# Optimization experiments

Measured on AMD Instinct MI355X. Metric: run time of the kernel, lower is better.

The kernel has to match this reference:

```python
import jax, jax.numpy as jnp
import numpy as np

SEQ, BATCH, IN_DIM, HID, OUT = 512, 256, 300, 256, 2


def setup_inputs() -> dict:
    key = jax.random.key(0)
    ks = jax.random.split(key, 7)
    s_ih = 1.0 / np.sqrt(HID)
    return {
        "x": jax.random.normal(ks[0], (SEQ, BATCH, IN_DIM), jnp.float32),
        "W_ih": jax.random.uniform(ks[1], (HID, IN_DIM), jnp.float32, -s_ih, s_ih),
        "W_hh": jax.random.uniform(ks[2], (HID, HID), jnp.float32, -s_ih, s_ih),
        "b_ih": jax.random.uniform(ks[3], (HID,), jnp.float32, -s_ih, s_ih),
        "b_hh": jax.random.uniform(ks[4], (HID,), jnp.float32, -s_ih, s_ih),
        "W_fc": jax.random.uniform(ks[5], (OUT, HID), jnp.float32, -s_ih, s_ih),
        "b_fc": jax.random.uniform(ks[6], (OUT,), jnp.float32, -s_ih, s_ih),
    }


def reference(x, W_ih, W_hh, b_ih, b_hh, W_fc, b_fc):
    # Precompute input projection for all timesteps at once: [T, B, H]
    xp = jnp.einsum('tbi,hi->tbh', x, W_ih) + b_ih + b_hh

    def step(h, xt):
        h_new = jnp.tanh(xt + h @ W_hh.T)
        return h_new, None

    h0 = jnp.zeros((x.shape[1], W_hh.shape[0]), x.dtype)
    hT, _ = jax.lax.scan(step, h0, xp)  # hT: [B, H]
    # Dropout(0.3) is identity in eval mode.
    logits = hT @ W_fc.T + b_fc  # [B, 2]
    return jax.nn.log_softmax(logits, axis=-1)
```

## Files before the change

### kernel.cpp

```cpp
#include <hip/hip_runtime.h>
#include <hip/hip_bf16.h>
#include <cstdint>
#include <cstddef>

#define SEQ 512
#define BATCH 256
#define IN_DIM 300
#define HID 256

typedef __attribute__((ext_vector_type(8))) short bf16x8;
typedef __attribute__((ext_vector_type(4))) float f32x4;

__device__ __forceinline__ unsigned short f2bf(float f) {
  union { float f; unsigned int u; } v; v.f = f;
  unsigned int u = v.u;
  return (unsigned short)((u + 0x7fffu + ((u >> 16) & 1u)) >> 16);
}
__device__ __forceinline__ unsigned short f2bf_fast(float f) {
  union { float f; unsigned int u; } v; v.f = f;
  return (unsigned short)((v.u + 0x8000u) >> 16);
}
__device__ __forceinline__ float bitsf(unsigned int u) {
  union { unsigned int u; float f; } v; v.u = u; return v.f;
}
__device__ __forceinline__ bf16x8 cvt8(float a0,float a1,float a2,float a3,
                                       float a4,float a5,float a6,float a7) {
  union { __hip_bfloat162 h2[4]; bf16x8 v; } c;
  c.h2[0] = __float22bfloat162_rn(make_float2(a0, a1));
  c.h2[1] = __float22bfloat162_rn(make_float2(a2, a3));
  c.h2[2] = __float22bfloat162_rn(make_float2(a4, a5));
  c.h2[3] = __float22bfloat162_rn(make_float2(a6, a7));
  return c.v;
}

__global__ __launch_bounds__(256) void conv_wih(const float* __restrict__ w,
                                                unsigned short* __restrict__ w_bf) {
  int idx = blockIdx.x * 256 + threadIdx.x;
  int n = idx / 320, k = idx - n * 320;
  float v = (k < IN_DIM) ? w[n * IN_DIM + k] : 0.f;
  w_bf[idx] = f2bf(v);
}

__global__ __launch_bounds__(256) void gemm_xp(const float* __restrict__ x,
    const unsigned short* __restrict__ w_bf, const float* __restrict__ b_ih,
    const float* __restrict__ b_hh, unsigned short* __restrict__ xp2)
{
  __shared__ unsigned short a_lds[64][40];
  __shared__ unsigned short w_lds[256][40];
  const int tid  = threadIdx.x;
  const int wave = tid >> 6;
  const int lane = tid & 63;
  const int l15  = lane & 15;
  const int quad = lane >> 4;
  const long m0 = (long)blockIdx.x * 64;

  f32x4 acc[4][4];
  #pragma unroll
  for (int mt = 0; mt < 4; ++mt)
    #pragma unroll
    for (int nt = 0; nt < 4; ++nt) acc[mt][nt] = (f32x4){0.f, 0.f, 0.f, 0.f};

  const int ar = tid >> 2;
  const int ac = (tid & 3) * 8;

  for (int kc = 0; kc < 10; ++kc) {
    const int k0 = kc * 32;
    {
      float v[8];
      const float* src = x + (size_t)(m0 + ar) * IN_DIM + (k0 + ac);
      if (k0 + ac + 8 <= IN_DIM) {
        float2 p0 = *(const float2*)(src + 0);
        float2 p1 = *(const float2*)(src + 2);
        float2 p2 = *(const float2*)(src + 4);
        float2 p3 = *(const float2*)(src + 6);
        v[0]=p0.x; v[1]=p0.y; v[2]=p1.x; v[3]=p1.y;
        v[4]=p2.x; v[5]=p2.y; v[6]=p3.x; v[7]=p3.y;
      } else {
        #pragma unroll
        for (int j = 0; j < 8; ++j) v[j] = (k0 + ac + j < IN_DIM) ? src[j] : 0.f;
      }
      *(bf16x8*)&a_lds[ar][ac] = cvt8(v[0],v[1],v[2],v[3],v[4],v[5],v[6],v[7]);
    }
    #pragma unroll
    for (int i = 0; i < 8; ++i) {
      int e = tid + i * 256;
      int n = e >> 3;
      int kk = (e & 7) * 4;
      uint2 d = *(const uint2*)(w_bf + n * 320 + k0 + kk);
      *(uint2*)&w_lds[n][kk] = d;
    }
    __syncthreads();
    bf16x8 afr[4], bfr[4];
    #pragma unroll
    for (int mt = 0; mt < 4; ++mt)
      afr[mt] = *(const bf16x8*)&a_lds[mt*16 + l15][quad*8];
    #pragma unroll
    for (int nt = 0; nt < 4; ++nt)
      bfr[nt] = *(const bf16x8*)&w_lds[wave*64 + nt*16 + l15][quad*8];
    #pragma unroll
    for (int mt = 0; mt < 4; ++mt)
      #pragma unroll
      for (int nt = 0; nt < 4; ++nt)
        acc[mt][nt] = __builtin_amdgcn_mfma_f32_16x16x32_bf16(afr[mt], bfr[nt], acc[mt][nt], 0, 0, 0);
    __syncthreads();
  }
  const int t = (int)(blockIdx.x >> 2);
  #pragma unroll
  for (int nt = 0; nt < 4; ++nt) {
    const int n = wave*64 + nt*16 + l15;
    const float kb = 2.0f * (b_ih[n] + b_hh[n]);
    const int tid_s = (wave*2 + (nt>>1))*64 + (nt&1)*32 + (quad&1)*16 + l15;
    #pragma unroll
    for (int mt = 0; mt < 4; ++mt) {
      const int g = ((int)(blockIdx.x & 3))*8 + mt*2 + (quad>>1);
      float y0 = fmaf(2.0f, acc[mt][nt][0], kb);
      float y1 = fmaf(2.0f, acc[mt][nt][1], kb);
      float y2 = fmaf(2.0f, acc[mt][nt][2], kb);
      float y3 = fmaf(2.0f, acc[mt][nt][3], kb);
      union { __hip_bfloat162 h2[2]; uint2 u; } pk;
      pk.h2[0] = __float22bfloat162_rn(make_float2(y0, y1));
      pk.h2[1] = __float22bfloat162_rn(make_float2(y2, y3));
      *(uint2*)(xp2 + (((size_t)t*32 + g)*512 + tid_s)*4) = pk.u;
    }
  }
}

__global__ __launch_bounds__(512) void rnn_scan(const float* __restrict__ W_hh,
    const unsigned short* __restrict__ xp2, float* __restrict__ hT)
{
  __shared__ unsigned short hbuf[2][8 * 264];
  const int tid  = threadIdx.x;
  const int wave = tid >> 6;
  const int lane = tid & 63;
  const int l15  = lane & 15;
  const int quad = lane >> 4;
  const int g = blockIdx.x;
  const int c0 = wave * 32;

  bf16x8 wf[2][8];
  #pragma unroll
  for (int nt = 0; nt < 2; ++nt) {
    const int n = c0 + nt*16 + l15;
    #pragma unroll
    for (int kc = 0; kc < 8; ++kc) {
      const float* src = W_hh + n*HID + kc*32 + quad*8;
      float4 p0 = *(const float4*)src;
      float4 p1 = *(const float4*)(src + 4);
      wf[nt][kc] = cvt8(p0.x,p0.y,p0.z,p0.w,p1.x,p1.y,p1.z,p1.w);
    }
  }

  const int myrow = ((lane >> 4) & 1) * 4;
  const int mycol = c0 + ((lane >> 5) << 4) + l15;
  const int b = g * 8 + myrow;

  for (int i = tid; i < 8 * 264; i += 512) hbuf[0][i] = 0;

  const unsigned short* xbase = xp2 + (((size_t)g) * 512 + tid) * 4;

  __syncthreads();

  uint2 xq[16];
  for (int tc = 0; tc < SEQ / 16; ++tc) {
    const unsigned short* pb = xbase + (size_t)tc * 16 * 65536;
    #pragma unroll
    for (int j = 0; j < 16; ++j)
      xq[j] = *(const uint2*)(pb + (size_t)j * 65536);
    #pragma unroll
    for (int j = 0; j < 16; ++j) {
      const int t = tc * 16 + j;
      const int cur = j & 1;
      bf16x8 afr[8];
      #pragma unroll
      for (int kc = 0; kc < 8; ++kc)
        afr[kc] = *(const bf16x8*)&hbuf[cur][(l15 & 7) * 264 + kc*32 + quad*8];
      f32x4 acc0 = (f32x4){0.f,0.f,0.f,0.f};
      f32x4 acc1 = (f32x4){0.f,0.f,0.f,0.f};
      #pragma unroll
      for (int kc = 0; kc < 8; ++kc) {
        acc0 = __builtin_amdgcn_mfma_f32_16x16x32_bf16(afr[kc], wf[0][kc], acc0, 0, 0, 0);
        acc1 = __builtin_amdgcn_mfma_f32_16x16x32_bf16(afr[kc], wf[1][kc], acc1, 0, 0, 0);
      }
      float xv[4];
      xv[0] = bitsf(xq[j].x << 16);
      xv[1] = bitsf(xq[j].x & 0xffff0000u);
      xv[2] = bitsf(xq[j].y << 16);
      xv[3] = bitsf(xq[j].y & 0xffff0000u);
      #pragma unroll
      for (int r = 0; r < 4; ++r) {
        float sel = (lane < 32) ? acc0[r] : acc1[r];
        float y  = fmaf(2.0f, sel, xv[r]);
        float e  = __expf(y);
        float hv = fmaf(-2.0f, __builtin_amdgcn_rcpf(e + 1.0f), 1.0f);
        if (t < SEQ - 1)
          hbuf[1 - cur][(myrow + r) * 264 + mycol] = f2bf_fast(hv);
        else
          hT[(size_t)(b + r) * HID + mycol] = hv;
      }
      __syncthreads();
    }
  }
}

__global__ __launch_bounds__(64) void fc_head(const float* __restrict__ hT,
    const float* __restrict__ W_fc, const float* __restrict__ b_fc,
    float* __restrict__ out)
{
  const int b = blockIdx.x;
  const int l = threadIdx.x;
  float s0 = 0.f, s1 = 0.f;
  #pragma unroll
  for (int j0 = 0; j0 < HID; j0 += 64) {
    float h = hT[(size_t)b * HID + j0 + l];
    s0 += h * W_fc[j0 + l];
    s1 += h * W_fc[HID + j0 + l];
  }
  #pragma unroll
  for (int off = 32; off > 0; off >>= 1) {
    s0 += __shfl_xor(s0, off, 64);
    s1 += __shfl_xor(s1, off, 64);
  }
  if (l == 0) {
    float l0 = s0 + b_fc[0], l1 = s1 + b_fc[1];
    float m = fmaxf(l0, l1);
    float lse = m + logf(expf(l0 - m) + expf(l1 - m));
    out[b*2 + 0] = l0 - lse;
    out[b*2 + 1] = l1 - lse;
  }
}

extern "C" void kernel_launch(void* const* d_in, const int* in_sizes, int n_in,
                              void* d_out, int out_size, void* d_ws, size_t ws_size,
                              hipStream_t stream) {
  const float* x    = (const float*)d_in[0];
  const float* W_ih = (const float*)d_in[1];
  const float* W_hh = (const float*)d_in[2];
  const float* b_ih = (const float*)d_in[3];
  const float* b_hh = (const float*)d_in[4];
  const float* W_fc = (const float*)d_in[5];
  const float* b_fc = (const float*)d_in[6];
  float* out = (float*)d_out;

  const size_t xp_bytes = (size_t)SEQ * BATCH * HID * 2;
  const size_t wb_bytes = (size_t)256 * 320 * 2;
  const size_t ht_bytes = (size_t)BATCH * HID * 4;
  if (ws_size < xp_bytes + wb_bytes + ht_bytes) return;

  char* ws = (char*)d_ws;
  unsigned short* xp2  = (unsigned short*)ws;
  unsigned short* w_bf = (unsigned short*)(ws + xp_bytes);
  float*          hT   = (float*)(ws + xp_bytes + wb_bytes);

  hipLaunchKernelGGL(conv_wih, dim3(320),  dim3(256), 0, stream, W_ih, w_bf);
  hipLaunchKernelGGL(gemm_xp,  dim3(2048), dim3(256), 0, stream, x, w_bf, b_ih, b_hh, xp2);
  hipLaunchKernelGGL(rnn_scan, dim3(32),   dim3(512), 0, stream, W_hh, xp2, hT);
  hipLaunchKernelGGL(fc_head,  dim3(BATCH), dim3(64), 0, stream, hT, W_fc, b_fc, out);
}
```

Before: 519.1 us.

## Split RNN scan across 64 blocks of 4 batch rows and prefetch GEMM tiles

The recurrent scan now runs 64 workgroups of 4 batch rows each instead of 32 of 8, so twice as many compute units share the serial recurrence. Each thread handles two hidden outputs instead of four, which shortens the per-step tail. The xp layout changes to match, and the MFMA chain is split into two independent accumulators to shorten dependency latency. The input-projection GEMM also register-prefetches the next K tile's global loads while computing the current one. MFMA rows 4-15 are now redundant padding, so matrix-core utilisation per step drops.

```diff
diff --git a/kernel.cpp b/kernel.cpp
--- a/kernel.cpp
+++ b/kernel.cpp
@@ -43,7 +43,7 @@
 
 __global__ __launch_bounds__(256) void gemm_xp(const float* __restrict__ x,
     const unsigned short* __restrict__ w_bf, const float* __restrict__ b_ih,
-    const float* __restrict__ b_hh, unsigned short* __restrict__ xp2)
+    const float* __restrict__ b_hh, unsigned int* __restrict__ xp2)
 {
   __shared__ unsigned short a_lds[64][40];
   __shared__ unsigned short w_lds[256][40];
@@ -63,33 +63,51 @@
   const int ar = tid >> 2;
   const int ac = (tid & 3) * 8;
 
+  float av[8];
+  uint2 wv[8];
+  {
+    const float* src = x + (size_t)(m0 + ar) * IN_DIM + ac;
+    float2 p0 = *(const float2*)(src + 0);
+    float2 p1 = *(const float2*)(src + 2);
+    float2 p2 = *(const float2*)(src + 4);
+    float2 p3 = *(const float2*)(src + 6);
+    av[0]=p0.x; av[1]=p0.y; av[2]=p1.x; av[3]=p1.y;
+    av[4]=p2.x; av[5]=p2.y; av[6]=p3.x; av[7]=p3.y;
+    #pragma unroll
+    for (int i = 0; i < 8; ++i) {
+      int e = tid + i * 256;
+      wv[i] = *(const uint2*)(w_bf + (e >> 3) * 320 + (e & 7) * 4);
+    }
+  }
+
   for (int kc = 0; kc < 10; ++kc) {
-    const int k0 = kc * 32;
-    {
-      float v[8];
+    *(bf16x8*)&a_lds[ar][ac] = cvt8(av[0],av[1],av[2],av[3],av[4],av[5],av[6],av[7]);
+    #pragma unroll
+    for (int i = 0; i < 8; ++i) {
+      int e = tid + i * 256;
+      *(uint2*)&w_lds[e >> 3][(e & 7) * 4] = wv[i];
+    }
+    __syncthreads();
+    if (kc < 9) {
+      const int k0 = (kc + 1) * 32;
       const float* src = x + (size_t)(m0 + ar) * IN_DIM + (k0 + ac);
       if (k0 + ac + 8 <= IN_DIM) {
         float2 p0 = *(const float2*)(src + 0);
         float2 p1 = *(const float2*)(src + 2);
         float2 p2 = *(const float2*)(src + 4);
         float2 p3 = *(const float2*)(src + 6);
-        v[0]=p0.x; v[1]=p0.y; v[2]=p1.x; v[3]=p1.y;
-        v[4]=p2.x; v[5]=p2.y; v[6]=p3.x; v[7]=p3.y;
+        av[0]=p0.x; av[1]=p0.y; av[2]=p1.x; av[3]=p1.y;
+        av[4]=p2.x; av[5]=p2.y; av[6]=p3.x; av[7]=p3.y;
       } else {
         #pragma unroll
-        for (int j = 0; j < 8; ++j) v[j] = (k0 + ac + j < IN_DIM) ? src[j] : 0.f;
-      }
-      *(bf16x8*)&a_lds[ar][ac] = cvt8(v[0],v[1],v[2],v[3],v[4],v[5],v[6],v[7]);
-    }
-    #pragma unroll
-    for (int i = 0; i < 8; ++i) {
-      int e = tid + i * 256;
-      int n = e >> 3;
-      int kk = (e & 7) * 4;
-      uint2 d = *(const uint2*)(w_bf + n * 320 + k0 + kk);
-      *(uint2*)&w_lds[n][kk] = d;
-    }
-    __syncthreads();
+        for (int j = 0; j < 8; ++j) av[j] = (k0 + ac + j < IN_DIM) ? src[j] : 0.f;
+      }
+      #pragma unroll
+      for (int i = 0; i < 8; ++i) {
+        int e = tid + i * 256;
+        wv[i] = *(const uint2*)(w_bf + (e >> 3) * 320 + k0 + (e & 7) * 4);
+      }
+    }
     bf16x8 afr[4], bfr[4];
     #pragma unroll
     for (int mt = 0; mt < 4; ++mt)
@@ -109,26 +127,28 @@
   for (int nt = 0; nt < 4; ++nt) {
     const int n = wave*64 + nt*16 + l15;
     const float kb = 2.0f * (b_ih[n] + b_hh[n]);
-    const int tid_s = (wave*2 + (nt>>1))*64 + (nt&1)*32 + (quad&1)*16 + l15;
+    const int tid_lo = (wave*2 + (nt>>1))*64 + (nt&1)*16 + l15;
     #pragma unroll
     for (int mt = 0; mt < 4; ++mt) {
-      const int g = ((int)(blockIdx.x & 3))*8 + mt*2 + (quad>>1);
+      const int g = ((int)(blockIdx.x & 3))*16 + mt*4 + quad;
+      const size_t base = ((size_t)t*64 + g)*512;
       float y0 = fmaf(2.0f, acc[mt][nt][0], kb);
       float y1 = fmaf(2.0f, acc[mt][nt][1], kb);
       float y2 = fmaf(2.0f, acc[mt][nt][2], kb);
       float y3 = fmaf(2.0f, acc[mt][nt][3], kb);
-      union { __hip_bfloat162 h2[2]; uint2 u; } pk;
-      pk.h2[0] = __float22bfloat162_rn(make_float2(y0, y1));
-      pk.h2[1] = __float22bfloat162_rn(make_float2(y2, y3));
-      *(uint2*)(xp2 + (((size_t)t*32 + g)*512 + tid_s)*4) = pk.u;
+      union { __hip_bfloat162 h2; unsigned int u; } p01, p23;
+      p01.h2 = __float22bfloat162_rn(make_float2(y0, y1));
+      p23.h2 = __float22bfloat162_rn(make_float2(y2, y3));
+      xp2[base + tid_lo]      = p01.u;
+      xp2[base + tid_lo + 32] = p23.u;
     }
   }
 }
 
 __global__ __launch_bounds__(512) void rnn_scan(const float* __restrict__ W_hh,
-    const unsigned short* __restrict__ xp2, float* __restrict__ hT)
+    const unsigned int* __restrict__ xp2, float* __restrict__ hT)
 {
-  __shared__ unsigned short hbuf[2][8 * 264];
+  __shared__ alignas(16) unsigned short hbuf[2][4 * 272];
   const int tid  = threadIdx.x;
   const int wave = tid >> 6;
   const int lane = tid & 63;
@@ -150,52 +170,54 @@
     }
   }
 
-  const int myrow = ((lane >> 4) & 1) * 4;
-  const int mycol = c0 + ((lane >> 5) << 4) + l15;
-  const int b = g * 8 + myrow;
-
-  for (int i = tid; i < 8 * 264; i += 512) hbuf[0][i] = 0;
-
-  const unsigned short* xbase = xp2 + (((size_t)g) * 512 + tid) * 4;
+  const int rb    = (quad >> 1) * 2;
+  const int col_e = c0 + (quad & 1) * 16 + l15;
+  const int abase = (l15 & 3) * 272 + quad * 8;
+
+  for (int i = tid; i < 4 * 272; i += 512) hbuf[0][i] = 0;
+
+  const unsigned int* xbase = xp2 + (size_t)g * 512 + tid;
 
   __syncthreads();
 
-  uint2 xq[16];
+  unsigned int xq[16];
   for (int tc = 0; tc < SEQ / 16; ++tc) {
-    const unsigned short* pb = xbase + (size_t)tc * 16 * 65536;
+    const unsigned int* pb = xbase + (size_t)tc * 16 * 32768;
     #pragma unroll
     for (int j = 0; j < 16; ++j)
-      xq[j] = *(const uint2*)(pb + (size_t)j * 65536);
+      xq[j] = pb[(size_t)j * 32768];
     #pragma unroll
     for (int j = 0; j < 16; ++j) {
-      const int t = tc * 16 + j;
       const int cur = j & 1;
       bf16x8 afr[8];
       #pragma unroll
       for (int kc = 0; kc < 8; ++kc)
-        afr[kc] = *(const bf16x8*)&hbuf[cur][(l15 & 7) * 264 + kc*32 + quad*8];
-      f32x4 acc0 = (f32x4){0.f,0.f,0.f,0.f};
-      f32x4 acc1 = (f32x4){0.f,0.f,0.f,0.f};
-      #pragma unroll
-      for (int kc = 0; kc < 8; ++kc) {
-        acc0 = __builtin_amdgcn_mfma_f32_16x16x32_bf16(afr[kc], wf[0][kc], acc0, 0, 0, 0);
-        acc1 = __builtin_amdgcn_mfma_f32_16x16x32_bf16(afr[kc], wf[1][kc], acc1, 0, 0, 0);
-      }
-      float xv[4];
-      xv[0] = bitsf(xq[j].x << 16);
-      xv[1] = bitsf(xq[j].x & 0xffff0000u);
-      xv[2] = bitsf(xq[j].y << 16);
-      xv[3] = bitsf(xq[j].y & 0xffff0000u);
-      #pragma unroll
-      for (int r = 0; r < 4; ++r) {
-        float sel = (lane < 32) ? acc0[r] : acc1[r];
-        float y  = fmaf(2.0f, sel, xv[r]);
-        float e  = __expf(y);
-        float hv = fmaf(-2.0f, __builtin_amdgcn_rcpf(e + 1.0f), 1.0f);
-        if (t < SEQ - 1)
-          hbuf[1 - cur][(myrow + r) * 264 + mycol] = f2bf_fast(hv);
-        else
-          hT[(size_t)(b + r) * HID + mycol] = hv;
+        afr[kc] = *(const bf16x8*)&hbuf[cur][abase + kc*32];
+      f32x4 a0A = (f32x4){0.f,0.f,0.f,0.f}, a0B = a0A, a1A = a0A, a1B = a0A;
+      #pragma unroll
+      for (int kc = 0; kc < 8; kc += 2) {
+        a0A = __builtin_amdgcn_mfma_f32_16x16x32_bf16(afr[kc],   wf[0][kc],   a0A, 0, 0, 0);
+        a1A = __builtin_amdgcn_mfma_f32_16x16x32_bf16(afr[kc],   wf[1][kc],   a1A, 0, 0, 0);
+        a0B = __builtin_amdgcn_mfma_f32_16x16x32_bf16(afr[kc+1], wf[0][kc+1], a0B, 0, 0, 0);
+        a1B = __builtin_amdgcn_mfma_f32_16x16x32_bf16(afr[kc+1], wf[1][kc+1], a1B, 0, 0, 0);
+      }
+      f32x4 acc0 = a0A + a0B;
+      f32x4 acc1 = a1A + a1B;
+      f32x4 a = (quad & 1) ? acc1 : acc0;
+      float s0 = (quad >> 1) ? a[2] : a[0];
+      float s1 = (quad >> 1) ? a[3] : a[1];
+      float xv0 = bitsf(xq[j] << 16);
+      float xv1 = bitsf(xq[j] & 0xffff0000u);
+      float y0 = fmaf(2.0f, s0, xv0);
+      float y1 = fmaf(2.0f, s1, xv1);
+      float h0 = fmaf(-2.0f, __builtin_amdgcn_rcpf(__expf(y0) + 1.0f), 1.0f);
+      float h1 = fmaf(-2.0f, __builtin_amdgcn_rcpf(__expf(y1) + 1.0f), 1.0f);
+      if (j < 15 || tc < SEQ/16 - 1) {
+        hbuf[1 - cur][ rb      * 272 + col_e] = f2bf_fast(h0);
+        hbuf[1 - cur][(rb + 1) * 272 + col_e] = f2bf_fast(h1);
+      } else {
+        hT[(size_t)(g*4 + rb    ) * HID + col_e] = h0;
+        hT[(size_t)(g*4 + rb + 1) * HID + col_e] = h1;
       }
       __syncthreads();
     }
@@ -247,12 +269,12 @@
   if (ws_size < xp_bytes + wb_bytes + ht_bytes) return;
 
   char* ws = (char*)d_ws;
-  unsigned short* xp2  = (unsigned short*)ws;
+  unsigned int*   xp2  = (unsigned int*)ws;
   unsigned short* w_bf = (unsigned short*)(ws + xp_bytes);
   float*          hT   = (float*)(ws + xp_bytes + wb_bytes);
 
   hipLaunchKernelGGL(conv_wih, dim3(320),  dim3(256), 0, stream, W_ih, w_bf);
   hipLaunchKernelGGL(gemm_xp,  dim3(2048), dim3(256), 0, stream, x, w_bf, b_ih, b_hh, xp2);
-  hipLaunchKernelGGL(rnn_scan, dim3(32),   dim3(512), 0, stream, W_hh, xp2, hT);
+  hipLaunchKernelGGL(rnn_scan, dim3(64),   dim3(512), 0, stream, W_hh, xp2, hT);
   hipLaunchKernelGGL(fc_head,  dim3(BATCH), dim3(64), 0, stream, hT, W_fc, b_fc, out);
 }
```

New measurement: 501.6 us. -3.4%, faster.
